# Kernel tuning notes

Measured on AMD Instinct MI355X. Metric: run time of the kernel, lower is better.

The kernel has to match this reference:

```python
import jax, jax.numpy as jnp
import numpy as np

N_NODES = 50000
IN_DIM = 64
OUT_DIM = 128
N_EDGES = 800000


def setup_inputs() -> dict:
    key = jax.random.key(0)
    k1, k2, k3, k4, k5 = jax.random.split(key, 5)
    x = jax.random.normal(k1, (N_NODES, IN_DIM), dtype=jnp.float32)
    edge_index = jax.random.randint(k2, (2, N_EDGES), 0, N_NODES, dtype=jnp.int64)
    # PyG SAGEConv params: lin_l (neighbor path, with bias), lin_r (root path, no bias)
    s = 1.0 / np.sqrt(IN_DIM)
    W_l = jax.random.uniform(k3, (OUT_DIM, IN_DIM), dtype=jnp.float32, minval=-s, maxval=s)
    b_l = jax.random.uniform(k4, (OUT_DIM,), dtype=jnp.float32, minval=-s, maxval=s)
    W_r = jax.random.uniform(k5, (OUT_DIM, IN_DIM), dtype=jnp.float32, minval=-s, maxval=s)
    return {"x": x, "edge_index": edge_index, "W_l": W_l, "b_l": b_l, "W_r": W_r}


def reference(x, edge_index, W_l, b_l, W_r):
    # Single-layer GraphSAGE (PyG SAGEConv, mean aggregation).
    # BasicGNN applies no activation after the last (only) layer.
    src = edge_index[0]  # message sources
    dst = edge_index[1]  # aggregation targets
    n = x.shape[0]
    # gather neighbor features and mean-aggregate per destination node
    summed = jax.ops.segment_sum(x[src], dst, num_segments=n)          # [N, IN_DIM]
    cnt = jax.ops.segment_sum(jnp.ones_like(src, dtype=x.dtype), dst, num_segments=n)
    mean = summed / jnp.clip(cnt, 1.0)[:, None]
    # out = lin_l(mean_neighbors) + lin_r(x)
    out = mean @ W_l.T + b_l + x @ W_r.T                               # [N, OUT_DIM]
    return out
```

## Files before the change

### kernel.cpp

```cpp
#include <hip/hip_runtime.h>

#define N_NODES 50000
#define IN_DIM 64
#define OUT_DIM 128
#define N_EDGES 800000

#define NPART 1024
#define EPP 782
#define NPLACE 256
#define NBUCK 391
#define WLDS 136
#define FIXSCALE 1048576.0f
#define INVFIX (1.0f / 1048576.0f)

typedef __attribute__((ext_vector_type(8))) short bf16x8;
typedef __attribute__((ext_vector_type(4))) float f32x4;

__device__ __forceinline__ unsigned short f2bf(float f) {
    unsigned u = __float_as_uint(f);
    unsigned r = u + 0x7FFFu + ((u >> 16) & 1u);
    return (unsigned short)(r >> 16);
}

__device__ __forceinline__ int SW(int nd, int f) { return (nd << 6) + (f ^ ((nd & 7) << 3)); }

__global__ __launch_bounds__(256) void p1_count_cvt(const int* __restrict__ ei,
                                                    const float* __restrict__ x,
                                                    const float* __restrict__ Wl,
                                                    const float* __restrict__ Wr,
                                                    int* __restrict__ cnt_mat,
                                                    unsigned short* __restrict__ xh,
                                                    unsigned short* __restrict__ w2h)
{
    __shared__ int h[NBUCK];
    int t = threadIdx.x, blk = blockIdx.x;
    for (int i = t; i < NBUCK; i += 256) h[i] = 0;
    __syncthreads();
    int s = blk * EPP;
    int e_end = min(s + EPP, N_EDGES);
    for (int i = s + t; i < e_end; i += 256)
        atomicAdd(&h[ei[N_EDGES + i] >> 7], 1);
    for (int gi = blk * 256 + t; gi < N_NODES * 16; gi += NPART * 256) {
        float4 v = ((const float4*)x)[gi];
        ushort4 o;
        o.x = f2bf(v.x); o.y = f2bf(v.y); o.z = f2bf(v.z); o.w = f2bf(v.w);
        ((ushort4*)xh)[gi] = o;
    }
    if (blk < 128 && t < 64) {
        w2h[blk * 128 + t]      = f2bf(Wr[blk * 64 + t]);
        w2h[blk * 128 + 64 + t] = f2bf(Wl[blk * 64 + t]);
    }
    __syncthreads();
    for (int b = t; b < NBUCK; b += 256) cnt_mat[b * NPART + blk] = h[b];
}

__global__ __launch_bounds__(256) void rowsum(const int* __restrict__ cnt_mat,
                                              int* __restrict__ tot)
{
    __shared__ int ws[4];
    int t = threadIdx.x, b = blockIdx.x;
    int lane = t & 63, w = t >> 6;
    int4 v = ((const int4*)(cnt_mat + b * NPART))[t];
    int sv = v.x + v.y + v.z + v.w;
#pragma unroll
    for (int d = 32; d >= 1; d >>= 1) sv += __shfl_down(sv, d, 64);
    if (lane == 0) ws[w] = sv;
    __syncthreads();
    if (t == 0) tot[b] = ws[0] + ws[1] + ws[2] + ws[3];
}

__global__ __launch_bounds__(256) void rowscan2(int* __restrict__ cnt_mat,
                                                const int* __restrict__ tot)
{
    __shared__ int bst_s;
    __shared__ int wtot[4];
    int t = threadIdx.x, b = blockIdx.x;
    int lane = t & 63, w = t >> 6;

    int4 mine = ((const int4*)(cnt_mat + b * NPART))[t];
    int s = mine.x + mine.y + mine.z + mine.w;
    int incl = s;
#pragma unroll
    for (int d = 1; d < 64; d <<= 1) {
        int u = __shfl_up(incl, d, 64);
        if (lane >= d) incl += u;
    }
    if (lane == 63) wtot[w] = incl;

    if (w == 0) {
        int carry = 0;
        for (int base = 0; base < NBUCK; base += 64) {
            int i = base + lane;
            int v = (i < NBUCK) ? tot[i] : 0;
            int ic = v;
#pragma unroll
            for (int d = 1; d < 64; d <<= 1) {
                int u = __shfl_up(ic, d, 64);
                if (lane >= d) ic += u;
            }
            if (i == b) bst_s = carry + ic - v;
            carry += __shfl(ic, 63, 64);
        }
    }
    __syncthreads();
    int woff = 0;
    for (int j = 0; j < w; ++j) woff += wtot[j];
    int base = bst_s + woff + incl - s;
    int4 outv;
    outv.x = base;
    outv.y = base + mine.x;
    outv.z = base + mine.x + mine.y;
    outv.w = base + mine.x + mine.y + mine.z;
    ((int4*)(cnt_mat + b * NPART))[t] = outv;
}

__global__ __launch_bounds__(256) void bucket_place(const int* __restrict__ ei,
                                                    const int* __restrict__ cnt_scan,
                                                    unsigned* __restrict__ ebuf)
{
    __shared__ int cur[NBUCK];
    int t = threadIdx.x, blk = blockIdx.x;
    for (int b = t; b < NBUCK; b += 256) cur[b] = cnt_scan[b * NPART + blk * 4];
    __syncthreads();
    int s = blk * 4 * EPP;
    int e_end = min(s + 4 * EPP, N_EDGES);
    for (int i = s + t; i < e_end; i += 256) {
        int src = ei[i], dst = ei[N_EDGES + i];
        int slot = atomicAdd(&cur[dst >> 7], 1);
        ebuf[slot] = (unsigned)src | ((unsigned)(dst & 127) << 16);
    }
}

__global__ __launch_bounds__(1024) void gather_mfma(const unsigned short* __restrict__ xh,
                                                    const int* __restrict__ cnt_scan,
                                                    const unsigned* __restrict__ ebuf,
                                                    const unsigned short* __restrict__ w2h,
                                                    const float* __restrict__ bl,
                                                    float* __restrict__ out)
{
    __shared__ int acc[128 * 64];
    __shared__ unsigned short wlds[128 * WLDS];
    __shared__ int dcnt[128];
    __shared__ int range_s[2];
    int t = threadIdx.x, b = blockIdx.x;
    int lane = t & 63, w = t >> 6;

#pragma unroll
    for (int c = 0; c < 2; ++c) {
        int idx = c * 1024 + t;
        int o = idx >> 4, kc = idx & 15;
        bf16x8 v = *(const bf16x8*)(w2h + o * 128 + kc * 8);
        *(bf16x8*)(&wlds[o * WLDS + kc * 8]) = v;
    }
    if (t == 0) {
        range_s[0] = cnt_scan[b * NPART];
        range_s[1] = (b < NBUCK - 1) ? cnt_scan[(b + 1) * NPART] : N_EDGES;
    }
#pragma unroll
    for (int i = 0; i < 8; ++i) acc[i * 1024 + t] = 0;
    if (t < 128) dcnt[t] = 0;
    __syncthreads();

    int bs = range_s[0], be = range_s[1];

    for (int e = bs + t; e < be; e += 1024)
        atomicAdd(&dcnt[(ebuf[e] >> 16) & 127], 1);

    for (int e0 = bs + w * 64; e0 < be; e0 += 1024) {
        int m = be - e0; if (m > 64) m = 64;
        unsigned pv = (lane < m) ? ebuf[e0 + lane] : 0u;
        for (int k = 0; k < m; k += 16) {
            unsigned p[16]; int fx[16];
#pragma unroll
            for (int u = 0; u < 16; ++u) p[u] = __shfl(pv, k + u, 64);
#pragma unroll
            for (int u = 0; u < 16; ++u) {
                unsigned short hv = xh[(size_t)(p[u] & 0xFFFFu) * IN_DIM + lane];
                fx[u] = __float2int_rn(__uint_as_float((unsigned)hv << 16) * FIXSCALE);
            }
#pragma unroll
            for (int u = 0; u < 16; ++u)
                if (k + u < m)
                    atomicAdd(&acc[SW((p[u] >> 16) & 127, lane)], fx[u]);
        }
    }
    __syncthreads();

    int s_strip = w & 7, hf = w >> 3;
    int nbase = b * 128 + s_strip * 16;
    if (nbase >= N_NODES) return;
    int row = lane & 15, q = lane >> 4;
    int nn = nbase + row;
    size_t nrow = (size_t)((nn < N_NODES) ? nn : (N_NODES - 1));

    bf16x8 a[4];
    a[0] = *(const bf16x8*)(xh + nrow * IN_DIM + q * 8);
    a[1] = *(const bf16x8*)(xh + nrow * IN_DIM + q * 8 + 32);

    int in_node = s_strip * 16 + row;
    int deg = dcnt[in_node];
    float sc = deg ? INVFIX / (float)deg : 0.0f;
    bf16x8 a2, a3;
#pragma unroll
    for (int j = 0; j < 8; ++j) {
        a2[j] = (short)f2bf((float)acc[SW(in_node, q * 8 + j)] * sc);
        a3[j] = (short)f2bf((float)acc[SW(in_node, 32 + q * 8 + j)] * sc);
    }
    a[2] = a2; a[3] = a3;

    f32x4 accf[4];
#pragma unroll
    for (int jj = 0; jj < 4; ++jj) accf[jj] = (f32x4){0.f, 0.f, 0.f, 0.f};

#pragma unroll
    for (int jj = 0; jj < 4; ++jj) {
        int ot = hf * 4 + jj;
        const unsigned short* wb = &wlds[(ot * 16 + row) * WLDS + q * 8];
#pragma unroll
        for (int s = 0; s < 4; ++s) {
            bf16x8 bfrag = *(const bf16x8*)(wb + s * 32);
            accf[jj] = __builtin_amdgcn_mfma_f32_16x16x32_bf16(a[s], bfrag, accf[jj], 0, 0, 0);
        }
    }

#pragma unroll
    for (int jj = 0; jj < 4; ++jj) {
        int ot = hf * 4 + jj;
        float bias = bl[ot * 16 + row];
#pragma unroll
        for (int r = 0; r < 4; ++r) {
            int n = nbase + q * 4 + r;
            if (n < N_NODES)
                out[(size_t)n * OUT_DIM + ot * 16 + row] = accf[jj][r] + bias;
        }
    }
}

extern "C" void kernel_launch(void* const* d_in, const int* in_sizes, int n_in,
                              void* d_out, int out_size, void* d_ws, size_t ws_size,
                              hipStream_t stream) {
    const float* x  = (const float*)d_in[0];
    const int*   ei = (const int*)d_in[1];
    const float* Wl = (const float*)d_in[2];
    const float* bl = (const float*)d_in[3];
    const float* Wr = (const float*)d_in[4];
    float* out = (float*)d_out;

    int*            cnt_mat = (int*)d_ws;
    int*            tot     = cnt_mat + NBUCK * NPART;
    unsigned*       ebuf    = (unsigned*)(tot + NBUCK + 1);
    unsigned short* xh      = (unsigned short*)(ebuf + N_EDGES);
    unsigned short* w2h     = xh + (size_t)N_NODES * IN_DIM;

    p1_count_cvt<<<NPART, 256, 0, stream>>>(ei, x, Wl, Wr, cnt_mat, xh, w2h);
    rowsum<<<NBUCK, 256, 0, stream>>>(cnt_mat, tot);
    rowscan2<<<NBUCK, 256, 0, stream>>>(cnt_mat, tot);
    bucket_place<<<NPLACE, 256, 0, stream>>>(ei, cnt_mat, ebuf);
    gather_mfma<<<NBUCK, 1024, 0, stream>>>(xh, cnt_mat, ebuf, w2h, bl, out);
}
```

Measured before the change: 73.83 us.

## Use 200-node buckets, fuse bucket totals into count pass, unroll gather

```diff
diff --git a/kernel.cpp b/kernel.cpp
--- a/kernel.cpp
+++ b/kernel.cpp
@@ -8,7 +8,8 @@
 #define NPART 1024
 #define EPP 782
 #define NPLACE 256
-#define NBUCK 391
+#define NBUCK 250
+#define NPB 200
 #define WLDS 136
 #define FIXSCALE 1048576.0f
 #define INVFIX (1.0f / 1048576.0f)
@@ -29,6 +30,7 @@
                                                     const float* __restrict__ Wl,
                                                     const float* __restrict__ Wr,
                                                     int* __restrict__ cnt_mat,
+                                                    int* __restrict__ tot,
                                                     unsigned short* __restrict__ xh,
                                                     unsigned short* __restrict__ w2h)
 {
@@ -39,7 +41,7 @@
     int s = blk * EPP;
     int e_end = min(s + EPP, N_EDGES);
     for (int i = s + t; i < e_end; i += 256)
-        atomicAdd(&h[ei[N_EDGES + i] >> 7], 1);
+        atomicAdd(&h[ei[N_EDGES + i] / NPB], 1);
     for (int gi = blk * 256 + t; gi < N_NODES * 16; gi += NPART * 256) {
         float4 v = ((const float4*)x)[gi];
         ushort4 o;
@@ -51,22 +53,10 @@
         w2h[blk * 128 + 64 + t] = f2bf(Wl[blk * 64 + t]);
     }
     __syncthreads();
-    for (int b = t; b < NBUCK; b += 256) cnt_mat[b * NPART + blk] = h[b];
-}
-
-__global__ __launch_bounds__(256) void rowsum(const int* __restrict__ cnt_mat,
-                                              int* __restrict__ tot)
-{
-    __shared__ int ws[4];
-    int t = threadIdx.x, b = blockIdx.x;
-    int lane = t & 63, w = t >> 6;
-    int4 v = ((const int4*)(cnt_mat + b * NPART))[t];
-    int sv = v.x + v.y + v.z + v.w;
-#pragma unroll
-    for (int d = 32; d >= 1; d >>= 1) sv += __shfl_down(sv, d, 64);
-    if (lane == 0) ws[w] = sv;
-    __syncthreads();
-    if (t == 0) tot[b] = ws[0] + ws[1] + ws[2] + ws[3];
+    for (int b = t; b < NBUCK; b += 256) {
+        cnt_mat[b * NPART + blk] = h[b];
+        if (h[b]) atomicAdd(&tot[b], h[b]);
+    }
 }
 
 __global__ __launch_bounds__(256) void rowscan2(int* __restrict__ cnt_mat,
@@ -89,8 +79,9 @@
 
     if (w == 0) {
         int carry = 0;
-        for (int base = 0; base < NBUCK; base += 64) {
-            int i = base + lane;
+#pragma unroll
+        for (int c = 0; c < 4; ++c) {
+            int i = c * 64 + lane;
             int v = (i < NBUCK) ? tot[i] : 0;
             int ic = v;
 #pragma unroll
@@ -126,8 +117,9 @@
     int e_end = min(s + 4 * EPP, N_EDGES);
     for (int i = s + t; i < e_end; i += 256) {
         int src = ei[i], dst = ei[N_EDGES + i];
-        int slot = atomicAdd(&cur[dst >> 7], 1);
-        ebuf[slot] = (unsigned)src | ((unsigned)(dst & 127) << 16);
+        int bkt = dst / NPB;
+        int slot = atomicAdd(&cur[bkt], 1);
+        ebuf[slot] = (unsigned)src | ((unsigned)(dst - bkt * NPB) << 16);
     }
 }
 
@@ -138,9 +130,9 @@
                                                     const float* __restrict__ bl,
                                                     float* __restrict__ out)
 {
-    __shared__ int acc[128 * 64];
+    __shared__ int acc[NPB * 64];
     __shared__ unsigned short wlds[128 * WLDS];
-    __shared__ int dcnt[128];
+    __shared__ int dcnt[NPB];
     __shared__ int range_s[2];
     int t = threadIdx.x, b = blockIdx.x;
     int lane = t & 63, w = t >> 6;
@@ -156,82 +148,95 @@
         range_s[0] = cnt_scan[b * NPART];
         range_s[1] = (b < NBUCK - 1) ? cnt_scan[(b + 1) * NPART] : N_EDGES;
     }
-#pragma unroll
-    for (int i = 0; i < 8; ++i) acc[i * 1024 + t] = 0;
-    if (t < 128) dcnt[t] = 0;
-    __syncthreads();
-
-    int bs = range_s[0], be = range_s[1];
+    for (int i = t; i < NPB * 64; i += 1024) acc[i] = 0;
+    if (t < NPB) dcnt[t] = 0;
+    __syncthreads();
+
+    int bs = __builtin_amdgcn_readfirstlane(range_s[0]);
+    int be = __builtin_amdgcn_readfirstlane(range_s[1]);
 
     for (int e = bs + t; e < be; e += 1024)
-        atomicAdd(&dcnt[(ebuf[e] >> 16) & 127], 1);
-
-    for (int e0 = bs + w * 64; e0 < be; e0 += 1024) {
+        atomicAdd(&dcnt[(ebuf[e] >> 16) & 255], 1);
+
+    int wu = __builtin_amdgcn_readfirstlane(w);
+    for (int e0 = bs + wu * 64; e0 < be; e0 += 1024) {
         int m = be - e0; if (m > 64) m = 64;
-        unsigned pv = (lane < m) ? ebuf[e0 + lane] : 0u;
-        for (int k = 0; k < m; k += 16) {
-            unsigned p[16]; int fx[16];
-#pragma unroll
-            for (int u = 0; u < 16; ++u) p[u] = __shfl(pv, k + u, 64);
-#pragma unroll
-            for (int u = 0; u < 16; ++u) {
-                unsigned short hv = xh[(size_t)(p[u] & 0xFFFFu) * IN_DIM + lane];
-                fx[u] = __float2int_rn(__uint_as_float((unsigned)hv << 16) * FIXSCALE);
-            }
-#pragma unroll
-            for (int u = 0; u < 16; ++u)
-                if (k + u < m)
-                    atomicAdd(&acc[SW((p[u] >> 16) & 127, lane)], fx[u]);
-        }
-    }
-    __syncthreads();
-
-    int s_strip = w & 7, hf = w >> 3;
-    int nbase = b * 128 + s_strip * 16;
-    if (nbase >= N_NODES) return;
+        if (m == 64) {
+#pragma unroll
+            for (int k = 0; k < 64; k += 16) {
+                unsigned p[16];
+#pragma unroll
+                for (int u = 0; u < 16; ++u) p[u] = ebuf[e0 + k + u];
+                int fx[16], sa[16];
+#pragma unroll
+                for (int u = 0; u < 16; ++u) {
+                    int src = (int)(p[u] & 0xFFFFu);
+                    unsigned short hv = xh[(size_t)src * IN_DIM + lane];
+                    fx[u] = __float2int_rn(__uint_as_float((unsigned)hv << 16) * FIXSCALE);
+                    int nd = (int)((p[u] >> 16) & 255u);
+                    sa[u] = SW(nd, lane);
+                }
+#pragma unroll
+                for (int u = 0; u < 16; ++u) atomicAdd(&acc[sa[u]], fx[u]);
+            }
+        } else {
+            for (int k = 0; k < m; ++k) {
+                unsigned p = ebuf[e0 + k];
+                int src = (int)(p & 0xFFFFu);
+                unsigned short hv = xh[(size_t)src * IN_DIM + lane];
+                int fx = __float2int_rn(__uint_as_float((unsigned)hv << 16) * FIXSCALE);
+                atomicAdd(&acc[SW((int)((p >> 16) & 255u), lane)], fx);
+            }
+        }
+    }
+    __syncthreads();
+
     int row = lane & 15, q = lane >> 4;
-    int nn = nbase + row;
-    size_t nrow = (size_t)((nn < N_NODES) ? nn : (N_NODES - 1));
-
-    bf16x8 a[4];
-    a[0] = *(const bf16x8*)(xh + nrow * IN_DIM + q * 8);
-    a[1] = *(const bf16x8*)(xh + nrow * IN_DIM + q * 8 + 32);
-
-    int in_node = s_strip * 16 + row;
-    int deg = dcnt[in_node];
-    float sc = deg ? INVFIX / (float)deg : 0.0f;
-    bf16x8 a2, a3;
-#pragma unroll
-    for (int j = 0; j < 8; ++j) {
-        a2[j] = (short)f2bf((float)acc[SW(in_node, q * 8 + j)] * sc);
-        a3[j] = (short)f2bf((float)acc[SW(in_node, 32 + q * 8 + j)] * sc);
-    }
-    a[2] = a2; a[3] = a3;
-
-    f32x4 accf[4];
-#pragma unroll
-    for (int jj = 0; jj < 4; ++jj) accf[jj] = (f32x4){0.f, 0.f, 0.f, 0.f};
-
-#pragma unroll
-    for (int jj = 0; jj < 4; ++jj) {
-        int ot = hf * 4 + jj;
-        const unsigned short* wb = &wlds[(ot * 16 + row) * WLDS + q * 8];
-#pragma unroll
-        for (int s = 0; s < 4; ++s) {
-            bf16x8 bfrag = *(const bf16x8*)(wb + s * 32);
-            accf[jj] = __builtin_amdgcn_mfma_f32_16x16x32_bf16(a[s], bfrag, accf[jj], 0, 0, 0);
-        }
-    }
-
-#pragma unroll
-    for (int jj = 0; jj < 4; ++jj) {
-        int ot = hf * 4 + jj;
-        float bias = bl[ot * 16 + row];
-#pragma unroll
-        for (int r = 0; r < 4; ++r) {
-            int n = nbase + q * 4 + r;
-            if (n < N_NODES)
-                out[(size_t)n * OUT_DIM + ot * 16 + row] = accf[jj][r] + bias;
+    for (int task = w; task < 26; task += 16) {
+        int strip = task >> 1, hf = task & 1;
+        int in_node = strip * 16 + row;
+        int in_c = (in_node < NPB) ? in_node : (NPB - 1);
+        size_t nrow = (size_t)(b * NPB + in_c);
+
+        bf16x8 a[4];
+        a[0] = *(const bf16x8*)(xh + nrow * IN_DIM + q * 8);
+        a[1] = *(const bf16x8*)(xh + nrow * IN_DIM + q * 8 + 32);
+
+        int deg = dcnt[in_c];
+        float sc = deg ? INVFIX / (float)deg : 0.0f;
+        bf16x8 a2, a3;
+#pragma unroll
+        for (int j = 0; j < 8; ++j) {
+            a2[j] = (short)f2bf((float)acc[SW(in_c, q * 8 + j)] * sc);
+            a3[j] = (short)f2bf((float)acc[SW(in_c, 32 + q * 8 + j)] * sc);
+        }
+        a[2] = a2; a[3] = a3;
+
+        f32x4 accf[4];
+#pragma unroll
+        for (int jj = 0; jj < 4; ++jj) accf[jj] = (f32x4){0.f, 0.f, 0.f, 0.f};
+
+#pragma unroll
+        for (int jj = 0; jj < 4; ++jj) {
+            int ot = hf * 4 + jj;
+            const unsigned short* wb = &wlds[(ot * 16 + row) * WLDS + q * 8];
+#pragma unroll
+            for (int s = 0; s < 4; ++s) {
+                bf16x8 bfrag = *(const bf16x8*)(wb + s * 32);
+                accf[jj] = __builtin_amdgcn_mfma_f32_16x16x32_bf16(a[s], bfrag, accf[jj], 0, 0, 0);
+            }
+        }
+
+#pragma unroll
+        for (int jj = 0; jj < 4; ++jj) {
+            int ot = hf * 4 + jj;
+            float bias = bl[ot * 16 + row];
+#pragma unroll
+            for (int r = 0; r < 4; ++r) {
+                int loc = strip * 16 + q * 4 + r;
+                if (loc < NPB)
+                    out[(size_t)(b * NPB + loc) * OUT_DIM + ot * 16 + row] = accf[jj][r] + bias;
+            }
         }
     }
 }
@@ -248,12 +253,12 @@
 
     int*            cnt_mat = (int*)d_ws;
     int*            tot     = cnt_mat + NBUCK * NPART;
-    unsigned*       ebuf    = (unsigned*)(tot + NBUCK + 1);
+    unsigned*       ebuf    = (unsigned*)(tot + 256);
     unsigned short* xh      = (unsigned short*)(ebuf + N_EDGES);
     unsigned short* w2h     = xh + (size_t)N_NODES * IN_DIM;
 
-    p1_count_cvt<<<NPART, 256, 0, stream>>>(ei, x, Wl, Wr, cnt_mat, xh, w2h);
-    rowsum<<<NBUCK, 256, 0, stream>>>(cnt_mat, tot);
+    hipMemsetAsync(tot, 0, 256 * sizeof(int), stream);
+    p1_count_cvt<<<NPART, 256, 0, stream>>>(ei, x, Wl, Wr, cnt_mat, tot, xh, w2h);
     rowscan2<<<NBUCK, 256, 0, stream>>>(cnt_mat, tot);
     bucket_place<<<NPLACE, 256, 0, stream>>>(ei, cnt_mat, ebuf);
     gather_mfma<<<NBUCK, 1024, 0, stream>>>(xh, cnt_mat, ebuf, w2h, bl, out);
```

After: 81.82 us. 10.8% more time.
